# Kernel tuning notes

Measured on AMD Instinct MI355X. Metric: run time of the kernel, lower is better.

Reference implementation:

```python
import jax, jax.numpy as jnp
import numpy as np
from jax import lax

B, H, W, C = 4, 96, 96, 256
F = 256
KH = KW = 3
K = KH * KW
DG = 1
CG = C // DG
SH = SW = 1
DH = DW = 1
PAD_T = (DH * (KH - 1)) // 2  # 'same' padding (top/left) for 3x3 dil 1
PAD_L = (DW * (KW - 1)) // 2


def setup_inputs() -> dict:
    key = jax.random.key(0)
    k1, k2, k3 = jax.random.split(key, 3)
    x = jax.random.normal(k1, (B, H, W, C), jnp.float32)
    # offset/mask conv weights (orig init zeros; small random to exercise sampling)
    om_kernel = jax.random.normal(k2, (KH, KW, C, DG * 3 * K), jnp.float32) * 0.01
    om_bias = jnp.zeros((DG * 3 * K,), jnp.float32)
    stdv = 1.0 / np.sqrt(C * KH * KW)
    kernel = jax.random.uniform(k3, (K * C, F), jnp.float32, -stdv, stdv)
    bias = jnp.zeros((F,), jnp.float32)
    return {"x": x, "om_kernel": om_kernel, "om_bias": om_bias, "kernel": kernel, "bias": bias}


def reference(x, om_kernel, om_bias, kernel, bias):
    Bx, Hx, Wx, Cx = x.shape
    # offset/mask prediction conv (NHWC, 'SAME', matches keras Conv2D)
    om = lax.conv_general_dilated(
        x, om_kernel, (SH, SW), "SAME", rhs_dilation=(DH, DW),
        dimension_numbers=("NHWC", "HWIO", "NHWC")) + om_bias
    Ho, Wo = om.shape[1], om.shape[2]
    off = om[..., : 2 * DG * K].reshape(Bx, Ho, Wo, DG, K, 2)  # (dy, dx) per group/kpoint
    mask = jax.nn.sigmoid(om[..., 2 * DG * K :]).reshape(Bx, Ho, Wo, DG, K) * 2.0

    # base sampling grid: y = ho*SH - PAD_T + ki*DH (+ dy), similarly x
    base_y = (jnp.arange(Ho) * SH - PAD_T)[:, None] + (jnp.arange(KH) * DH)[None, :]  # [Ho,KH]
    base_x = (jnp.arange(Wo) * SW - PAD_L)[:, None] + (jnp.arange(KW) * DW)[None, :]  # [Wo,KW]
    gy = jnp.broadcast_to(base_y[:, None, :, None], (Ho, Wo, KH, KW)).reshape(Ho, Wo, K)
    gx = jnp.broadcast_to(base_x[None, :, None, :], (Ho, Wo, KH, KW)).reshape(Ho, Wo, K)

    py = gy[None, :, :, None, :].astype(x.dtype) + off[..., 0]  # [B,Ho,Wo,DG,K]
    px = gx[None, :, :, None, :].astype(x.dtype) + off[..., 1]

    # reorder to [B, N, DG] with N = Ho*Wo*K (K varies fastest after spatial)
    N = Ho * Wo * K
    py = py.transpose(0, 1, 2, 4, 3).reshape(Bx, N, DG)
    px = px.transpose(0, 1, 2, 4, 3).reshape(Bx, N, DG)
    mask_t = mask.transpose(0, 1, 2, 4, 3).reshape(Bx, N, DG)

    y0 = jnp.floor(py)
    x0 = jnp.floor(px)
    fy = py - y0
    fx = px - x0

    xf = x.reshape(Bx, Hx * Wx, DG, CG)
    val = jnp.zeros((Bx, N, DG, CG), x.dtype)
    for yi, wy in ((y0, 1.0 - fy), (y0 + 1.0, fy)):
        for xi, wx in ((x0, 1.0 - fx), (x0 + 1.0, fx)):
            valid = (yi >= 0) & (yi < Hx) & (xi >= 0) & (xi < Wx)
            yc = jnp.clip(yi, 0, Hx - 1).astype(jnp.int32)
            xc = jnp.clip(xi, 0, Wx - 1).astype(jnp.int32)
            lin = yc * Wx + xc  # [B,N,DG]
            g = jnp.take_along_axis(xf, lin[..., None], axis=1)  # [B,N,DG,CG]
            val = val + g * (wy * wx * valid.astype(x.dtype))[..., None]

    # modulate and im2col -> GEMM
    cols = (val * mask_t[..., None]).reshape(Bx, Ho * Wo, K * Cx)
    out = jnp.matmul(cols, kernel).reshape(Bx, Ho, Wo, -1) + bias
    return out
```

## Files before the change

kernel.cpp:

```cpp
#include <hip/hip_runtime.h>
#include <hip/hip_bf16.h>
#include <stdint.h>
#include <stddef.h>


namespace {
constexpr int H  = 96, W = 96, C = 256, F = 256;
constexpr int HP = 98;
constexpr int NP = 4 * 96 * 96;
constexpr int KC = 9 * 256;

constexpr int NB_PAD  = 4 * HP * HP / 8;
constexpr int NB_OMW  = 9 * 32;
constexpr int NB_WT   = (KC / 64) * (F / 64);
constexpr int NB_ZERO = NP * 32 * 4 / 4096;
}

typedef __attribute__((ext_vector_type(8))) short bf16x8;
typedef __attribute__((ext_vector_type(4))) float floatx4;

__device__ __forceinline__ void load_lds16(const void* g, void* l) {
  __builtin_amdgcn_global_load_lds((const __attribute__((address_space(1))) void*)g,
                                   (__attribute__((address_space(3))) void*)l,
                                   16, 0, 0);
}

__device__ __forceinline__ uint32_t pk2(float lo, float hi) {
  __hip_bfloat162 t = __float22bfloat162_rn(float2{lo, hi});
  return *reinterpret_cast<uint32_t*>(&t);
}

__device__ __forceinline__ void acc8(uint4 v, float w, float* a) {
  a[0] += w * __uint_as_float(v.x << 16); a[1] += w * __uint_as_float(v.x & 0xffff0000u);
  a[2] += w * __uint_as_float(v.y << 16); a[3] += w * __uint_as_float(v.y & 0xffff0000u);
  a[4] += w * __uint_as_float(v.z << 16); a[5] += w * __uint_as_float(v.z & 0xffff0000u);
  a[6] += w * __uint_as_float(v.w << 16); a[7] += w * __uint_as_float(v.w & 0xffff0000u);
}

__global__ __launch_bounds__(256) void k_prep(const float* __restrict__ x,
                                              const float* __restrict__ omk,
                                              const float* __restrict__ kern,
                                              uint4* __restrict__ xp4,
                                              __hip_bfloat16* __restrict__ wom,
                                              __hip_bfloat16* __restrict__ wt,
                                              float4* __restrict__ pOmz) {
  __shared__ float t[64][65];
  const int bi = blockIdx.x, tid = threadIdx.x;

  if (bi < NB_PAD) {
    const int sub = tid >> 5, cid = tid & 31;
    const int pp  = bi * 8 + sub;
    const int b   = pp / (HP * HP);
    const int r   = pp % (HP * HP);
    const int y   = r / HP, xq = r % HP;
    uint4 o = {0u, 0u, 0u, 0u};
    if (y >= 1 && y <= H && xq >= 1 && xq <= W) {
      const float* src = x + ((size_t)((b * H + (y - 1)) * W + (xq - 1))) * C + cid * 8;
      const float4 v0 = *(const float4*)src;
      const float4 v1 = *(const float4*)(src + 4);
      o.x = pk2(v0.x, v0.y); o.y = pk2(v0.z, v0.w);
      o.z = pk2(v1.x, v1.y); o.w = pk2(v1.z, v1.w);
    }
    xp4[(size_t)pp * 32 + cid] = o;
  } else if (bi < NB_PAD + NB_OMW) {
    const int i  = bi - NB_PAD;
    const int kk = i / 32, oc = i % 32;
    float v = (oc < 27) ? omk[(size_t)(kk * 256 + tid) * 27 + oc] : 0.f;
    wom[(size_t)oc * KC + kk * 256 + tid] = __float2bfloat16(v);
  } else if (bi < NB_PAD + NB_OMW + NB_WT) {
    const int j   = bi - NB_PAD - NB_OMW;
    const int kc0 = (j % (KC / 64)) * 64, f0 = (j / (KC / 64)) * 64;
    const int rr = tid >> 6, cc = tid & 63;
#pragma unroll
    for (int i = 0; i < 16; ++i)
      t[rr * 16 + i][cc] = kern[(size_t)(kc0 + rr * 16 + i) * F + f0 + cc];
    __syncthreads();
#pragma unroll
    for (int i = 0; i < 16; ++i) {
      const int frow = rr * 16 + i;
      wt[(size_t)(f0 + frow) * KC + kc0 + cc] = __float2bfloat16(t[cc][frow]);
    }
  } else {
    const int j = bi - NB_PAD - NB_OMW - NB_WT;
    pOmz[(size_t)j * 256 + tid] = (float4){0.f, 0.f, 0.f, 0.f};
  }
}

__global__ __launch_bounds__(256) void k_omgemm(const __hip_bfloat16* __restrict__ xp,
                                                const __hip_bfloat16* __restrict__ wom,
                                                float* __restrict__ pOm) {
  __shared__ __align__(16) char lds[10240];
  const int tid  = threadIdx.x;
  const int m0   = blockIdx.x * 128;
  const int s    = blockIdx.y;
  const int lane = tid & 63, wave = tid >> 6;
  const int quad = lane >> 4, l16 = lane & 15;

  const int kp = (tid & 3) ^ ((tid >> 3) & 3);
  const __hip_bfloat16* abase[2];
#pragma unroll
  for (int j = 0; j < 2; ++j) {
    const int row = (tid >> 2) + j * 64;
    const int p = m0 + row;
    const int b = p / (H * W);
    const int hw = p % (H * W);
    const int h = hw / W, w = hw % W;
    abase[j] = xp + ((size_t)(b * HP + h) * HP + w) * C + kp * 8;
  }
  const __hip_bfloat16* bbase = wom + (size_t)(tid >> 2) * KC + kp * 8;

  floatx4 acc[2][2];
#pragma unroll
  for (int i = 0; i < 2; ++i)
#pragma unroll
    for (int j = 0; j < 2; ++j) acc[i][j] = (floatx4){0.f, 0.f, 0.f, 0.f};

  const int swq = (quad ^ ((l16 >> 1) & 3)) * 16;

  const int kbeg = s * 384;
#pragma unroll 1
  for (int k0 = kbeg; k0 < kbeg + 384; k0 += 32) {
    const int kk = k0 >> 8;
    const int c0 = k0 & 255;
    const int kh = kk / 3, kw = kk % 3;
    const int aoff = (kh * HP + kw) * C + c0;

    __syncthreads();
    load_lds16(abase[0] + aoff, &lds[tid * 16]);
    load_lds16(abase[1] + aoff, &lds[4096 + tid * 16]);
    if (tid < 128) load_lds16(bbase + k0, &lds[8192 + tid * 16]);
    __syncthreads();

    bf16x8 af[2], bfr[2];
#pragma unroll
    for (int mt = 0; mt < 2; ++mt)
      af[mt] = *(const bf16x8*)&lds[(wave * 32 + mt * 16 + l16) * 64 + swq];
#pragma unroll
    for (int nt = 0; nt < 2; ++nt)
      bfr[nt] = *(const bf16x8*)&lds[8192 + (nt * 16 + l16) * 64 + swq];
#pragma unroll
    for (int mt = 0; mt < 2; ++mt)
#pragma unroll
      for (int nt = 0; nt < 2; ++nt)
        acc[mt][nt] = __builtin_amdgcn_mfma_f32_16x16x32_bf16(af[mt], bfr[nt], acc[mt][nt], 0, 0, 0);
  }

#pragma unroll
  for (int mt = 0; mt < 2; ++mt)
#pragma unroll
    for (int nt = 0; nt < 2; ++nt) {
      const int gm = m0 + wave * 32 + mt * 16 + quad * 4;
      const int gn = nt * 16 + l16;
#pragma unroll
      for (int r = 0; r < 4; ++r)
        __hip_atomic_fetch_add(&pOm[(size_t)(gm + r) * 32 + gn], acc[mt][nt][r],
                               __ATOMIC_RELAXED, __HIP_MEMORY_SCOPE_AGENT);
    }
}

__global__ __launch_bounds__(256) void k_sample(const uint4* __restrict__ xp4,
                                                const float* __restrict__ pOm,
                                                const float* __restrict__ om_bias,
                                                uint4* __restrict__ cols4) {
  __shared__ float2 s_ow[8][9][4];

  const int tid = threadIdx.x;
  const int sub = tid >> 5, cid = tid & 31;

  if (tid < 72) {
    const int ps = tid / 9, k = tid % 9;
    const int p  = blockIdx.x * 8 + ps;
    const int b  = p / (H * W);
    const int hw = p % (H * W);
    const int h = hw / W, w = hw % W;
    const float dy = om_bias[2 * k]     + pOm[(size_t)p * 32 + 2 * k];
    const float dx = om_bias[2 * k + 1] + pOm[(size_t)p * 32 + 2 * k + 1];
    const float mv = om_bias[18 + k]    + pOm[(size_t)p * 32 + 18 + k];
    const float m  = 2.f / (1.f + __expf(-mv));
    const float sy = (float)(h - 1 + k / 3) + dy;
    const float sx = (float)(w - 1 + k % 3) + dx;
    const float y0f = floorf(sy), x0f = floorf(sx);
    const float fy = sy - y0f, fx = sx - x0f;
    const int y0 = (int)y0f, x0 = (int)x0f;
#pragma unroll
    for (int c2 = 0; c2 < 4; ++c2) {
      const int dy2 = c2 >> 1, dx2 = c2 & 1;
      const int yi = y0 + dy2, xi = x0 + dx2;
      const bool valid = (yi >= 0) & (yi < H) & (xi >= 0) & (xi < W);
      const float wgt = valid ? (dy2 ? fy : 1.f - fy) * (dx2 ? fx : 1.f - fx) * m : 0.f;
      const int yc = min(max(yi + 1, 0), HP - 1);
      const int xc = min(max(xi + 1, 0), HP - 1);
      const int off = ((b * HP + yc) * HP + xc) * 32;
      s_ow[ps][k][c2] = float2{__int_as_float(off), wgt};
    }
  }
  __syncthreads();

  const int p = blockIdx.x * 8 + sub;
  uint4* __restrict__ ob = cols4 + (size_t)p * 288 + cid;

#pragma unroll 1
  for (int k = 0; k < 9; ++k) {
    const float2 ow0 = s_ow[sub][k][0], ow1 = s_ow[sub][k][1];
    const float2 ow2 = s_ow[sub][k][2], ow3 = s_ow[sub][k][3];
    float a[8] = {0.f, 0.f, 0.f, 0.f, 0.f, 0.f, 0.f, 0.f};
    acc8(xp4[(size_t)__float_as_int(ow0.x) + cid], ow0.y, a);
    acc8(xp4[(size_t)__float_as_int(ow1.x) + cid], ow1.y, a);
    acc8(xp4[(size_t)__float_as_int(ow2.x) + cid], ow2.y, a);
    acc8(xp4[(size_t)__float_as_int(ow3.x) + cid], ow3.y, a);
    uint4 o;
    o.x = pk2(a[0], a[1]); o.y = pk2(a[2], a[3]);
    o.z = pk2(a[4], a[5]); o.w = pk2(a[6], a[7]);
    ob[k * 32] = o;
  }
}

__global__ __launch_bounds__(256) void k_gemm(const __hip_bfloat16* __restrict__ A,
                                              const __hip_bfloat16* __restrict__ Bt,
                                              const float* __restrict__ bias,
                                              float* __restrict__ out) {
  __shared__ __align__(16) char lds[14336];

  const int tid  = threadIdx.x;
  const int m0   = blockIdx.x * 96;
  const int n0   = blockIdx.y * 128;
  const int lane = tid & 63, wave = tid >> 6;
  const int wm = wave & 1, wn = wave >> 1;
  const int quad = lane >> 4, l16 = lane & 15;

  floatx4 acc[3][4];
#pragma unroll
  for (int i = 0; i < 3; ++i)
#pragma unroll
    for (int j = 0; j < 4; ++j) acc[i][j] = (floatx4){0.f, 0.f, 0.f, 0.f};

  const int swq = (quad ^ ((l16 >> 1) & 3)) * 16;

#pragma unroll 1
  for (int k0 = 0; k0 < KC; k0 += 32) {
    __syncthreads();
    {
      const int row = tid >> 2, kp = (tid & 3) ^ ((tid >> 3) & 3);
      load_lds16(A + (size_t)(m0 + row) * KC + k0 + kp * 8, &lds[tid * 16]);
      if (tid < 128)
        load_lds16(A + (size_t)(m0 + 64 + row) * KC + k0 + kp * 8, &lds[4096 + tid * 16]);
      load_lds16(Bt + (size_t)(n0 + row) * KC + k0 + kp * 8, &lds[6144 + tid * 16]);
      load_lds16(Bt + (size_t)(n0 + 64 + row) * KC + k0 + kp * 8, &lds[10240 + tid * 16]);
    }
    __syncthreads();

    bf16x8 af[3], bfr[4];
#pragma unroll
    for (int mt = 0; mt < 3; ++mt)
      af[mt] = *(const bf16x8*)&lds[(wm * 48 + mt * 16 + l16) * 64 + swq];
#pragma unroll
    for (int nt = 0; nt < 4; ++nt)
      bfr[nt] = *(const bf16x8*)&lds[6144 + (wn * 64 + nt * 16 + l16) * 64 + swq];
#pragma unroll
    for (int mt = 0; mt < 3; ++mt)
#pragma unroll
      for (int nt = 0; nt < 4; ++nt)
        acc[mt][nt] = __builtin_amdgcn_mfma_f32_16x16x32_bf16(af[mt], bfr[nt], acc[mt][nt], 0, 0, 0);
  }

#pragma unroll
  for (int mt = 0; mt < 3; ++mt) {
#pragma unroll
    for (int nt = 0; nt < 4; ++nt) {
      const int gm = m0 + wm * 48 + mt * 16 + quad * 4;
      const int gn = n0 + wn * 64 + nt * 16 + l16;
      const float bs = bias[gn];
#pragma unroll
      for (int r = 0; r < 4; ++r)
        out[(size_t)(gm + r) * F + gn] = acc[mt][nt][r] + bs;
    }
  }
}

extern "C" void kernel_launch(void* const* d_in, const int* in_sizes, int n_in,
                              void* d_out, int out_size, void* d_ws, size_t ws_size,
                              hipStream_t stream) {
  const float* x    = (const float*)d_in[0];
  const float* omk  = (const float*)d_in[1];
  const float* omb  = (const float*)d_in[2];
  const float* kern = (const float*)d_in[3];
  const float* bias = (const float*)d_in[4];
  float* out = (float*)d_out;

  char* ws = (char*)d_ws;
  size_t off = 0;
  __hip_bfloat16* wt   = (__hip_bfloat16*)(ws + off); off += (size_t)F * KC * 2;
  __hip_bfloat16* xp   = (__hip_bfloat16*)(ws + off); off += (size_t)4 * HP * HP * C * 2;
  __hip_bfloat16* wom  = (__hip_bfloat16*)(ws + off); off += (size_t)32 * KC * 2;
  float*          pOm  = (float*)(ws + off);          off += (size_t)NP * 32 * 4;
  __hip_bfloat16* cols = (__hip_bfloat16*)(ws + off);

  k_prep  <<<dim3(NB_PAD + NB_OMW + NB_WT + NB_ZERO), 256, 0, stream>>>(
      x, omk, kern, (uint4*)xp, wom, wt, (float4*)pOm);
  k_omgemm<<<dim3(NP / 128, 6),      256, 0, stream>>>(xp, wom, pOm);
  k_sample<<<dim3(NP / 8),           256, 0, stream>>>((const uint4*)xp, pOm, omb, (uint4*)cols);
  k_gemm  <<<dim3(NP / 96, F / 128), 256, 0, stream>>>(cols, wt, bias, out);
}
```

Baseline: 227.7 us.

## Fuse deformable bilinear sampling into the main GEMM, dropping the cols buffer

Merges the sampling kernel and the im2col GEMM into one kernel. Each 512-thread block computes 128 output pixels by all 256 filters, and gathers the bilinearly sampled, mask-modulated A tile straight into LDS for each 32-channel K slice. This avoids writing and re-reading the large bf16 cols matrix in global memory and saves one launch. In exchange, gather latency now sits inside the GEMM loop with no double buffering, each K step needs two barriers, and the grid shrinks to 144 blocks, which may underfill the GPU.

```diff
diff --git a/kernel.cpp b/kernel.cpp
--- a/kernel.cpp
+++ b/kernel.cpp
@@ -158,117 +158,107 @@
     }
 }
 
-__global__ __launch_bounds__(256) void k_sample(const uint4* __restrict__ xp4,
-                                                const float* __restrict__ pOm,
-                                                const float* __restrict__ om_bias,
-                                                uint4* __restrict__ cols4) {
-  __shared__ float2 s_ow[8][9][4];
-
-  const int tid = threadIdx.x;
-  const int sub = tid >> 5, cid = tid & 31;
-
-  if (tid < 72) {
-    const int ps = tid / 9, k = tid % 9;
-    const int p  = blockIdx.x * 8 + ps;
-    const int b  = p / (H * W);
-    const int hw = p % (H * W);
-    const int h = hw / W, w = hw % W;
-    const float dy = om_bias[2 * k]     + pOm[(size_t)p * 32 + 2 * k];
-    const float dx = om_bias[2 * k + 1] + pOm[(size_t)p * 32 + 2 * k + 1];
-    const float mv = om_bias[18 + k]    + pOm[(size_t)p * 32 + 18 + k];
-    const float m  = 2.f / (1.f + __expf(-mv));
-    const float sy = (float)(h - 1 + k / 3) + dy;
-    const float sx = (float)(w - 1 + k % 3) + dx;
-    const float y0f = floorf(sy), x0f = floorf(sx);
-    const float fy = sy - y0f, fx = sx - x0f;
-    const int y0 = (int)y0f, x0 = (int)x0f;
-#pragma unroll
-    for (int c2 = 0; c2 < 4; ++c2) {
-      const int dy2 = c2 >> 1, dx2 = c2 & 1;
+__global__ __launch_bounds__(512) void k_fused(const uint4* __restrict__ xp4,
+                                               const __hip_bfloat16* __restrict__ wt,
+                                               const float* __restrict__ pOm,
+                                               const float* __restrict__ omb,
+                                               const float* __restrict__ bias,
+                                               float* __restrict__ out) {
+  __shared__ __align__(16) char lds[28672];
+  float2* s_ow = (float2*)&lds[24576];
+
+  const int tid  = threadIdx.x;
+  const int m0   = blockIdx.x * 128;
+  const int lane = tid & 63, wave = tid >> 6;
+  const int wm = wave >> 2, wn = wave & 3;
+  const int quad = lane >> 4, l16 = lane & 15;
+  const int swq  = (quad ^ ((l16 >> 1) & 3)) * 16;
+
+  const int spx = tid >> 2, sq = tid & 3;
+  const int p_my  = m0 + spx;
+  const int b_my  = p_my / (H * W);
+  const int hw_my = p_my % (H * W);
+  const int h_my  = hw_my / W, w_my = hw_my % W;
+
+  const int bkp = (tid & 3) ^ ((tid >> 3) & 3);
+  const __hip_bfloat16* bsrc0 = wt + (size_t)(tid >> 2) * KC + bkp * 8;
+  const __hip_bfloat16* bsrc1 = bsrc0 + (size_t)128 * KC;
+
+  floatx4 acc[4][4];
+#pragma unroll
+  for (int i = 0; i < 4; ++i)
+#pragma unroll
+    for (int j = 0; j < 4; ++j) acc[i][j] = (floatx4){0.f, 0.f, 0.f, 0.f};
+
+#pragma unroll 1
+  for (int kk = 0; kk < 9; ++kk) {
+    {
+      const float dy = omb[2 * kk]     + pOm[(size_t)p_my * 32 + 2 * kk];
+      const float dx = omb[2 * kk + 1] + pOm[(size_t)p_my * 32 + 2 * kk + 1];
+      const float mv = omb[18 + kk]    + pOm[(size_t)p_my * 32 + 18 + kk];
+      const float m  = 2.f / (1.f + __expf(-mv));
+      const float sy = (float)(h_my - 1 + kk / 3) + dy;
+      const float sx = (float)(w_my - 1 + kk % 3) + dx;
+      const float y0f = floorf(sy), x0f = floorf(sx);
+      const float fy = sy - y0f, fx = sx - x0f;
+      const int y0 = (int)y0f, x0 = (int)x0f;
+      const int dy2 = sq >> 1, dx2 = sq & 1;
       const int yi = y0 + dy2, xi = x0 + dx2;
       const bool valid = (yi >= 0) & (yi < H) & (xi >= 0) & (xi < W);
       const float wgt = valid ? (dy2 ? fy : 1.f - fy) * (dx2 ? fx : 1.f - fx) * m : 0.f;
       const int yc = min(max(yi + 1, 0), HP - 1);
       const int xc = min(max(xi + 1, 0), HP - 1);
-      const int off = ((b * HP + yc) * HP + xc) * 32;
-      s_ow[ps][k][c2] = float2{__int_as_float(off), wgt};
-    }
-  }
-  __syncthreads();
-
-  const int p = blockIdx.x * 8 + sub;
-  uint4* __restrict__ ob = cols4 + (size_t)p * 288 + cid;
+      const int off = ((b_my * HP + yc) * HP + xc) * 32;
+      s_ow[spx * 4 + sq] = float2{__int_as_float(off), wgt};
+    }
+    __syncthreads();
+
+    const float4 ow01 = *(const float4*)&s_ow[spx * 4 + 0];
+    const float4 ow23 = *(const float4*)&s_ow[spx * 4 + 2];
+    const uint4* p0 = xp4 + __float_as_int(ow01.x) + sq;
+    const uint4* p1 = xp4 + __float_as_int(ow01.z) + sq;
+    const uint4* p2 = xp4 + __float_as_int(ow23.x) + sq;
+    const uint4* p3 = xp4 + __float_as_int(ow23.z) + sq;
+    const float w0 = ow01.y, w1 = ow01.w, w2 = ow23.y, w3 = ow23.w;
 
 #pragma unroll 1
-  for (int k = 0; k < 9; ++k) {
-    const float2 ow0 = s_ow[sub][k][0], ow1 = s_ow[sub][k][1];
-    const float2 ow2 = s_ow[sub][k][2], ow3 = s_ow[sub][k][3];
-    float a[8] = {0.f, 0.f, 0.f, 0.f, 0.f, 0.f, 0.f, 0.f};
-    acc8(xp4[(size_t)__float_as_int(ow0.x) + cid], ow0.y, a);
-    acc8(xp4[(size_t)__float_as_int(ow1.x) + cid], ow1.y, a);
-    acc8(xp4[(size_t)__float_as_int(ow2.x) + cid], ow2.y, a);
-    acc8(xp4[(size_t)__float_as_int(ow3.x) + cid], ow3.y, a);
-    uint4 o;
-    o.x = pk2(a[0], a[1]); o.y = pk2(a[2], a[3]);
-    o.z = pk2(a[4], a[5]); o.w = pk2(a[6], a[7]);
-    ob[k * 32] = o;
-  }
-}
-
-__global__ __launch_bounds__(256) void k_gemm(const __hip_bfloat16* __restrict__ A,
-                                              const __hip_bfloat16* __restrict__ Bt,
-                                              const float* __restrict__ bias,
-                                              float* __restrict__ out) {
-  __shared__ __align__(16) char lds[14336];
-
-  const int tid  = threadIdx.x;
-  const int m0   = blockIdx.x * 96;
-  const int n0   = blockIdx.y * 128;
-  const int lane = tid & 63, wave = tid >> 6;
-  const int wm = wave & 1, wn = wave >> 1;
-  const int quad = lane >> 4, l16 = lane & 15;
-
-  floatx4 acc[3][4];
-#pragma unroll
-  for (int i = 0; i < 3; ++i)
-#pragma unroll
-    for (int j = 0; j < 4; ++j) acc[i][j] = (floatx4){0.f, 0.f, 0.f, 0.f};
-
-  const int swq = (quad ^ ((l16 >> 1) & 3)) * 16;
-
-#pragma unroll 1
-  for (int k0 = 0; k0 < KC; k0 += 32) {
-    __syncthreads();
-    {
-      const int row = tid >> 2, kp = (tid & 3) ^ ((tid >> 3) & 3);
-      load_lds16(A + (size_t)(m0 + row) * KC + k0 + kp * 8, &lds[tid * 16]);
-      if (tid < 128)
-        load_lds16(A + (size_t)(m0 + 64 + row) * KC + k0 + kp * 8, &lds[4096 + tid * 16]);
-      load_lds16(Bt + (size_t)(n0 + row) * KC + k0 + kp * 8, &lds[6144 + tid * 16]);
-      load_lds16(Bt + (size_t)(n0 + 64 + row) * KC + k0 + kp * 8, &lds[10240 + tid * 16]);
-    }
-    __syncthreads();
-
-    bf16x8 af[3], bfr[4];
-#pragma unroll
-    for (int mt = 0; mt < 3; ++mt)
-      af[mt] = *(const bf16x8*)&lds[(wm * 48 + mt * 16 + l16) * 64 + swq];
-#pragma unroll
-    for (int nt = 0; nt < 4; ++nt)
-      bfr[nt] = *(const bf16x8*)&lds[6144 + (wn * 64 + nt * 16 + l16) * 64 + swq];
-#pragma unroll
-    for (int mt = 0; mt < 3; ++mt)
+    for (int c = 0; c < 8; ++c) {
+      load_lds16(bsrc0 + kk * 256 + c * 32, &lds[8192 + tid * 16]);
+      load_lds16(bsrc1 + kk * 256 + c * 32, &lds[16384 + tid * 16]);
+
+      const uint4 g0 = p0[c * 4], g1 = p1[c * 4], g2 = p2[c * 4], g3 = p3[c * 4];
+      float a[8] = {0.f, 0.f, 0.f, 0.f, 0.f, 0.f, 0.f, 0.f};
+      acc8(g0, w0, a); acc8(g1, w1, a); acc8(g2, w2, a); acc8(g3, w3, a);
+      uint4 o;
+      o.x = pk2(a[0], a[1]); o.y = pk2(a[2], a[3]);
+      o.z = pk2(a[4], a[5]); o.w = pk2(a[6], a[7]);
+      *(uint4*)&lds[spx * 64 + (sq ^ ((spx >> 1) & 3)) * 16] = o;
+
+      __syncthreads();
+
+      bf16x8 af[4], bfr[4];
+#pragma unroll
+      for (int mt = 0; mt < 4; ++mt)
+        af[mt] = *(const bf16x8*)&lds[(wm * 64 + mt * 16 + l16) * 64 + swq];
 #pragma unroll
       for (int nt = 0; nt < 4; ++nt)
-        acc[mt][nt] = __builtin_amdgcn_mfma_f32_16x16x32_bf16(af[mt], bfr[nt], acc[mt][nt], 0, 0, 0);
-  }
-
-#pragma unroll
-  for (int mt = 0; mt < 3; ++mt) {
+        bfr[nt] = *(const bf16x8*)&lds[8192 + (wn * 64 + nt * 16 + l16) * 64 + swq];
+#pragma unroll
+      for (int mt = 0; mt < 4; ++mt)
+#pragma unroll
+        for (int nt = 0; nt < 4; ++nt)
+          acc[mt][nt] = __builtin_amdgcn_mfma_f32_16x16x32_bf16(af[mt], bfr[nt], acc[mt][nt], 0, 0, 0);
+
+      __syncthreads();
+    }
+  }
+
+#pragma unroll
+  for (int mt = 0; mt < 4; ++mt) {
 #pragma unroll
     for (int nt = 0; nt < 4; ++nt) {
-      const int gm = m0 + wm * 48 + mt * 16 + quad * 4;
-      const int gn = n0 + wn * 64 + nt * 16 + l16;
+      const int gm = m0 + wm * 64 + mt * 16 + quad * 4;
+      const int gn = wn * 64 + nt * 16 + l16;
       const float bs = bias[gn];
 #pragma unroll
       for (int r = 0; r < 4; ++r)
@@ -293,11 +283,9 @@
   __hip_bfloat16* xp   = (__hip_bfloat16*)(ws + off); off += (size_t)4 * HP * HP * C * 2;
   __hip_bfloat16* wom  = (__hip_bfloat16*)(ws + off); off += (size_t)32 * KC * 2;
   float*          pOm  = (float*)(ws + off);          off += (size_t)NP * 32 * 4;
-  __hip_bfloat16* cols = (__hip_bfloat16*)(ws + off);
 
   k_prep  <<<dim3(NB_PAD + NB_OMW + NB_WT + NB_ZERO), 256, 0, stream>>>(
       x, omk, kern, (uint4*)xp, wom, wt, (float4*)pOm);
-  k_omgemm<<<dim3(NP / 128, 6),      256, 0, stream>>>(xp, wom, pOm);
-  k_sample<<<dim3(NP / 8),           256, 0, stream>>>((const uint4*)xp, pOm, omb, (uint4*)cols);
-  k_gemm  <<<dim3(NP / 96, F / 128), 256, 0, stream>>>(cols, wt, bias, out);
-}
+  k_omgemm<<<dim3(NP / 128, 6), 256, 0, stream>>>(xp, wom, pOm);
+  k_fused <<<dim3(NP / 128),    512, 0, stream>>>((const uint4*)xp, wt, pOm, omb, bias, out);
+}
```

New measurement: 305.8 us. 34.3% more time.

## Double-buffer LDS staging in GEMM kernels and remap blocks across XCDs

Applied to the files above, without the earlier changes.

Both the offset-conv GEMM and the main GEMM now use two LDS buffers. The next K-slice's global-to-LDS loads are issued right after the barrier, before the MFMAs on the current slice, which drops one barrier per iteration and overlaps memory traffic with compute. The offset GEMM and the sampling kernel also permute block indices, so consecutive tiles land on the same XCD for better L2 locality. LDS use doubles, which may lower occupancy.

```diff
diff --git a/kernel.cpp b/kernel.cpp
--- a/kernel.cpp
+++ b/kernel.cpp
@@ -89,9 +89,11 @@
 __global__ __launch_bounds__(256) void k_omgemm(const __hip_bfloat16* __restrict__ xp,
                                                 const __hip_bfloat16* __restrict__ wom,
                                                 float* __restrict__ pOm) {
-  __shared__ __align__(16) char lds[10240];
+  __shared__ __align__(16) char lds[20480];
   const int tid  = threadIdx.x;
-  const int m0   = blockIdx.x * 128;
+  const int xr   = blockIdx.x;
+  const int xs   = (xr & 7) * 36 + (xr >> 3);
+  const int m0   = xs * 128;
   const int s    = blockIdx.y;
   const int lane = tid & 63, wave = tid >> 6;
   const int quad = lane >> 4, l16 = lane & 15;
@@ -109,6 +111,15 @@
   }
   const __hip_bfloat16* bbase = wom + (size_t)(tid >> 2) * KC + kp * 8;
 
+  auto stage = [&](int buf, int k0) {
+    const int kk = k0 >> 8, c0 = k0 & 255;
+    const int aoff = ((kk / 3) * HP + (kk % 3)) * C + c0;
+    char* base = &lds[buf * 10240];
+    load_lds16(abase[0] + aoff, base + tid * 16);
+    load_lds16(abase[1] + aoff, base + 4096 + tid * 16);
+    if (tid < 128) load_lds16(bbase + k0, base + 8192 + tid * 16);
+  };
+
   floatx4 acc[2][2];
 #pragma unroll
   for (int i = 0; i < 2; ++i)
@@ -117,32 +128,28 @@
 
   const int swq = (quad ^ ((l16 >> 1) & 3)) * 16;
 
-  const int kbeg = s * 384;
+  const int kbeg = s * 384, kend = kbeg + 384;
+  stage(0, kbeg);
+  int cur = 0;
 #pragma unroll 1
-  for (int k0 = kbeg; k0 < kbeg + 384; k0 += 32) {
-    const int kk = k0 >> 8;
-    const int c0 = k0 & 255;
-    const int kh = kk / 3, kw = kk % 3;
-    const int aoff = (kh * HP + kw) * C + c0;
-
+  for (int k0 = kbeg; k0 < kend; k0 += 32) {
     __syncthreads();
-    load_lds16(abase[0] + aoff, &lds[tid * 16]);
-    load_lds16(abase[1] + aoff, &lds[4096 + tid * 16]);
-    if (tid < 128) load_lds16(bbase + k0, &lds[8192 + tid * 16]);
-    __syncthreads();
+    if (k0 + 32 < kend) stage(cur ^ 1, k0 + 32);
+    const char* base = &lds[cur * 10240];
 
     bf16x8 af[2], bfr[2];
 #pragma unroll
     for (int mt = 0; mt < 2; ++mt)
-      af[mt] = *(const bf16x8*)&lds[(wave * 32 + mt * 16 + l16) * 64 + swq];
+      af[mt] = *(const bf16x8*)&base[(wave * 32 + mt * 16 + l16) * 64 + swq];
 #pragma unroll
     for (int nt = 0; nt < 2; ++nt)
-      bfr[nt] = *(const bf16x8*)&lds[8192 + (nt * 16 + l16) * 64 + swq];
+      bfr[nt] = *(const bf16x8*)&base[8192 + (nt * 16 + l16) * 64 + swq];
 #pragma unroll
     for (int mt = 0; mt < 2; ++mt)
 #pragma unroll
       for (int nt = 0; nt < 2; ++nt)
         acc[mt][nt] = __builtin_amdgcn_mfma_f32_16x16x32_bf16(af[mt], bfr[nt], acc[mt][nt], 0, 0, 0);
+    cur ^= 1;
   }
 
 #pragma unroll
@@ -166,10 +173,11 @@
 
   const int tid = threadIdx.x;
   const int sub = tid >> 5, cid = tid & 31;
+  const int bs  = (blockIdx.x & 7) * 576 + (blockIdx.x >> 3);
 
   if (tid < 72) {
     const int ps = tid / 9, k = tid % 9;
-    const int p  = blockIdx.x * 8 + ps;
+    const int p  = bs * 8 + ps;
     const int b  = p / (H * W);
     const int hw = p % (H * W);
     const int h = hw / W, w = hw % W;
@@ -196,7 +204,7 @@
   }
   __syncthreads();
 
-  const int p = blockIdx.x * 8 + sub;
+  const int p = bs * 8 + sub;
   uint4* __restrict__ ob = cols4 + (size_t)p * 288 + cid;
 
 #pragma unroll 1
@@ -219,7 +227,7 @@
                                               const __hip_bfloat16* __restrict__ Bt,
                                               const float* __restrict__ bias,
                                               float* __restrict__ out) {
-  __shared__ __align__(16) char lds[14336];
+  __shared__ __align__(16) char lds[28672];
 
   const int tid  = threadIdx.x;
   const int m0   = blockIdx.x * 96;
@@ -228,6 +236,20 @@
   const int wm = wave & 1, wn = wave >> 1;
   const int quad = lane >> 4, l16 = lane & 15;
 
+  const int row = tid >> 2, kp = (tid & 3) ^ ((tid >> 3) & 3);
+  const __hip_bfloat16* a0 = A  + (size_t)(m0 + row) * KC + kp * 8;
+  const __hip_bfloat16* a1 = A  + (size_t)(m0 + 64 + row) * KC + kp * 8;
+  const __hip_bfloat16* b0 = Bt + (size_t)(n0 + row) * KC + kp * 8;
+  const __hip_bfloat16* b1 = Bt + (size_t)(n0 + 64 + row) * KC + kp * 8;
+
+  auto stage = [&](int buf, int k0) {
+    char* base = &lds[buf * 14336];
+    load_lds16(a0 + k0, base + tid * 16);
+    if (tid < 128) load_lds16(a1 + k0, base + 4096 + tid * 16);
+    load_lds16(b0 + k0, base + 6144 + tid * 16);
+    load_lds16(b1 + k0, base + 10240 + tid * 16);
+  };
+
   floatx4 acc[3][4];
 #pragma unroll
   for (int i = 0; i < 3; ++i)
@@ -236,31 +258,27 @@
 
   const int swq = (quad ^ ((l16 >> 1) & 3)) * 16;
 
+  stage(0, 0);
+  int cur = 0;
 #pragma unroll 1
   for (int k0 = 0; k0 < KC; k0 += 32) {
     __syncthreads();
-    {
-      const int row = tid >> 2, kp = (tid & 3) ^ ((tid >> 3) & 3);
-      load_lds16(A + (size_t)(m0 + row) * KC + k0 + kp * 8, &lds[tid * 16]);
-      if (tid < 128)
-        load_lds16(A + (size_t)(m0 + 64 + row) * KC + k0 + kp * 8, &lds[4096 + tid * 16]);
-      load_lds16(Bt + (size_t)(n0 + row) * KC + k0 + kp * 8, &lds[6144 + tid * 16]);
-      load_lds16(Bt + (size_t)(n0 + 64 + row) * KC + k0 + kp * 8, &lds[10240 + tid * 16]);
-    }
-    __syncthreads();
+    if (k0 + 32 < KC) stage(cur ^ 1, k0 + 32);
+    const char* base = &lds[cur * 14336];
 
     bf16x8 af[3], bfr[4];
 #pragma unroll
     for (int mt = 0; mt < 3; ++mt)
-      af[mt] = *(const bf16x8*)&lds[(wm * 48 + mt * 16 + l16) * 64 + swq];
+      af[mt] = *(const bf16x8*)&base[(wm * 48 + mt * 16 + l16) * 64 + swq];
 #pragma unroll
     for (int nt = 0; nt < 4; ++nt)
-      bfr[nt] = *(const bf16x8*)&lds[6144 + (wn * 64 + nt * 16 + l16) * 64 + swq];
+      bfr[nt] = *(const bf16x8*)&base[6144 + (wn * 64 + nt * 16 + l16) * 64 + swq];
 #pragma unroll
     for (int mt = 0; mt < 3; ++mt)
 #pragma unroll
       for (int nt = 0; nt < 4; ++nt)
         acc[mt][nt] = __builtin_amdgcn_mfma_f32_16x16x32_bf16(af[mt], bfr[nt], acc[mt][nt], 0, 0, 0);
+    cur ^= 1;
   }
 
 #pragma unroll
```

After: 222.0 us. 2.5% less time.
